# Optimization experiments

Hardware: AMD Instinct MI355X
Metric: run time of the kernel (lower is better)

Reference implementation:

```python
import jax, jax.numpy as jnp
import numpy as np

H_DIM = 2048
N_HEADS = 16

def setup_inputs() -> dict:
    key = jax.random.key(0)
    ks = jax.random.split(key, 9)
    B, T, C = 2, 2048, H_DIM
    scale = 1.0 / np.sqrt(C)  # lecun_normal approx
    src = jax.random.normal(ks[0], (B, T, C), dtype=jnp.float32)
    Wq = jax.random.normal(ks[1], (C, H_DIM), dtype=jnp.float32) * scale
    Wk = jax.random.normal(ks[2], (C, H_DIM), dtype=jnp.float32) * scale
    Wv = jax.random.normal(ks[3], (C, H_DIM), dtype=jnp.float32) * scale
    Wo = jax.random.normal(ks[4], (H_DIM, H_DIM), dtype=jnp.float32) * scale
    bq = jnp.zeros((H_DIM,), jnp.float32)
    bk = jnp.zeros((H_DIM,), jnp.float32)
    bv = jnp.zeros((H_DIM,), jnp.float32)
    bo = jnp.zeros((H_DIM,), jnp.float32)
    return {"src": src, "Wq": Wq, "bq": bq, "Wk": Wk, "bk": bk,
            "Wv": Wv, "bv": bv, "Wo": Wo, "bo": bo}

def reference(src, Wq, bq, Wk, bk, Wv, bv, Wo, bo):
    B, T, C = src.shape
    N = N_HEADS
    D = C // N
    def heads(x):  # [B,T,h_dim] -> [B,N,T,D]
        return x.reshape(B, T, N, D).transpose(0, 2, 1, 3)
    q = heads(src @ Wq + bq)
    k = heads(src @ Wk + bk)
    v = heads(src @ Wv + bv)
    # scaled dot-product with causal mask
    scores = jnp.einsum('bntd,bnsd->bnts', q, k) / jnp.sqrt(jnp.float32(D))
    causal = jnp.tril(jnp.ones((T, T), dtype=bool))
    scores = jnp.where(causal[None, None], scores, -jnp.inf)
    attn = jax.nn.softmax(scores, axis=-1)
    out = jnp.einsum('bnts,bnsd->bntd', attn, v)  # dropout is identity (drop_p=0)
    out = out.transpose(0, 2, 1, 3).reshape(B, T, N * D)
    return out @ Wo + bo
```

## Files before the change

kernel.cpp:

```cpp
#include <hip/hip_runtime.h>
#include <hip/hip_bf16.h>

typedef float f32x4 __attribute__((ext_vector_type(4)));
typedef __bf16 bf16x8v __attribute__((ext_vector_type(8)));
typedef __bf16 bf16x4v __attribute__((ext_vector_type(4)));
typedef unsigned uint2v __attribute__((ext_vector_type(2)));
typedef bf16x8v __attribute__((may_alias)) bf16x8;
typedef bf16x4v __attribute__((may_alias)) bf16x4;
typedef uint2v __attribute__((may_alias)) u32x2;

typedef __attribute__((address_space(1))) const void gvoid_t;
typedef __attribute__((address_space(3))) void lvoid_t;

#define DEVINL __device__ __forceinline__

#define BDIM 2
#define TDIM 2048
#define CDIM 2048
#define NHEAD 16
#define DHEAD 128
#define MROWS 4096
#define WSZ ((size_t)CDIM * CDIM)
#define XSZ ((size_t)MROWS * CDIM)

#define BARRIER_LGKM() asm volatile("s_waitcnt lgkmcnt(0)\ns_barrier" ::: "memory")

#define GEMM_BAR_LGKM()                              \
  do {                                               \
    asm volatile("s_waitcnt lgkmcnt(0)" ::: "memory"); \
    __builtin_amdgcn_sched_barrier(0);               \
    __builtin_amdgcn_s_barrier();                    \
  } while (0)

#define GEMM_BAR_VM(N)                                \
  do {                                                \
    asm volatile("s_waitcnt vmcnt(" #N ")" ::: "memory"); \
    __builtin_amdgcn_sched_barrier(0);                \
    __builtin_amdgcn_s_barrier();                     \
  } while (0)

DEVINL __bf16 f2bf(float f) {
  unsigned u = __builtin_bit_cast(unsigned, f);
  u += 0x7fffu + ((u >> 16) & 1u);
  unsigned short h = (unsigned short)(u >> 16);
  return __builtin_bit_cast(__bf16, h);
}

DEVINL unsigned pk2bf_trunc(float lo, float hi) {
  return __builtin_amdgcn_perm(__builtin_bit_cast(unsigned, hi),
                               __builtin_bit_cast(unsigned, lo), 0x07060302);
}

DEVINL void gl2lds16(const void* g, void* l) {
  __builtin_amdgcn_global_load_lds((gvoid_t*)g, (lvoid_t*)l, 16, 0, 0);
}

__global__ void detect_dtype(const unsigned* __restrict__ w,
                             int* __restrict__ flag, int* __restrict__ cnt) {
  const int l = threadIdx.x;
  if (l == 0) *cnt = 0;
  const unsigned word = w[l];
  const unsigned e = (word >> 7) & 0xFFu;
  const int vote = (e >= 0x70u && e <= 0x87u) ? 1 : 0;
  const unsigned long long m = __ballot(vote);
  if (l == 0) *flag = (__popcll(m) >= 32) ? 1 : 0;
}

__global__ __launch_bounds__(256) void cvt_src(const void* __restrict__ in,
                                               __bf16* __restrict__ out,
                                               const int* __restrict__ flag,
                                               int n8) {
  const int i = blockIdx.x * 256 + threadIdx.x;
  if (i >= n8) return;
  if (*flag) {
    ((bf16x8*)out)[i] = ((const bf16x8*)in)[i];
  } else {
    const float* f = (const float*)in + (size_t)i * 8;
    bf16x8v v;
#pragma unroll
    for (int j = 0; j < 8; ++j) v[j] = f2bf(f[j]);
    ((bf16x8*)out)[i] = v;
  }
}

__global__ __launch_bounds__(256) void cvt_wt(
    const void* __restrict__ w0, const void* __restrict__ w1,
    const void* __restrict__ w2, const void* __restrict__ w3,
    __bf16* __restrict__ out, const int* __restrict__ flag) {
  __shared__ __attribute__((aligned(16))) __bf16 tile[64][68];
  const void* W = (blockIdx.z == 0) ? w0 : (blockIdx.z == 1) ? w1
                : (blockIdx.z == 2) ? w2 : w3;
  __bf16* Wt = out + (size_t)blockIdx.z * WSZ;
  const int tx = threadIdx.x & 63, ty = threadIdx.x >> 6;
  const int k0 = blockIdx.x * 64, n0 = blockIdx.y * 64;
  const int fl = *flag;
#pragma unroll
  for (int i = ty; i < 64; i += 4) {
    const size_t off = (size_t)(k0 + i) * CDIM + n0 + tx;
    const float v = fl ? (float)((const __bf16*)W)[off] : ((const float*)W)[off];
    tile[i][tx] = f2bf(v);
  }
  __syncthreads();
#pragma unroll
  for (int i = ty; i < 64; i += 4)
    Wt[(size_t)(n0 + i) * CDIM + k0 + tx] = tile[tx][i];
}

__global__ __launch_bounds__(256) void cvt_bias(
    const void* __restrict__ b0, const void* __restrict__ b1,
    const void* __restrict__ b2, const void* __restrict__ b3,
    float* __restrict__ out, const int* __restrict__ flag) {
  const int i = blockIdx.x * 256 + threadIdx.x;
  const void* b = (i < 2048) ? b0 : (i < 4096) ? b1 : (i < 6144) ? b2 : b3;
  const int idx = i & 2047;
  out[i] = (*flag) ? (float)((const __bf16*)b)[idx] : ((const float*)b)[idx];
}

template <int NTN, int MODE>
__global__ __launch_bounds__(512, 2) void gemm8p(
    const __bf16* __restrict__ A, const __bf16* __restrict__ Bt,
    const float* __restrict__ bias, __bf16* __restrict__ qb,
    __bf16* __restrict__ kb, __bf16* __restrict__ vtb,
    const int* __restrict__ flag, void* __restrict__ outp) {
  constexpr int K = CDIM;
  constexpr int NKT = K / 64;
  __shared__ __attribute__((aligned(16))) __bf16 Als[2][128 * 64];
  __shared__ __attribute__((aligned(16))) __bf16 Bls[2][256 * 64];

  const int tid = threadIdx.x;
  const int w = tid >> 6, l = tid & 63;
  const int quad = l >> 4, l16 = l & 15;
  const int wm = (w >> 2) * 64, wn = (w & 3) * 64;

  const int bid = blockIdx.x;
  const int xcd = bid & 7, loc = bid >> 3;
  const int bm = loc & 31, bn = xcd * (NTN / 8) + (loc >> 5);
  const int m0 = bm * 128, n0 = bn * 256;

  const int srow = tid >> 3;
  const int scb = (tid & 7) ^ (srow & 7);
  const __bf16* gA = A + (size_t)(m0 + srow) * K + scb * 8;
  const __bf16* gB = Bt + (size_t)(n0 + srow) * K + scb * 8;
  const int wl = w * 512;

  const int aoff = (wm + l16) * 64;
  const int boff = (wn + l16) * 64;
  int cp[2];
  cp[0] = ((0 + quad) ^ (l16 & 7)) * 8;
  cp[1] = ((4 + quad) ^ (l16 & 7)) * 8;

  f32x4 acc[4][4];
#pragma unroll
  for (int i = 0; i < 4; ++i)
#pragma unroll
    for (int j = 0; j < 4; ++j) acc[i][j] = (f32x4){0.f, 0.f, 0.f, 0.f};

  gl2lds16(gA, &Als[0][wl]);
  gl2lds16(gA + (size_t)64 * K, &Als[0][4096 + wl]);
  gl2lds16(gB, &Bls[0][wl]);
  gl2lds16(gB + (size_t)64 * K, &Bls[0][4096 + wl]);
  gl2lds16(gB + (size_t)128 * K, &Bls[0][8192 + wl]);
  gl2lds16(gB + (size_t)192 * K, &Bls[0][12288 + wl]);
  gl2lds16(gA + 64, &Als[1][wl]);
  gl2lds16(gA + (size_t)64 * K + 64, &Als[1][4096 + wl]);

#define READ_HALF(I0)                                                        \
  _Pragma("unroll") for (int ii = 0; ii < 2; ++ii)                           \
  _Pragma("unroll") for (int ks = 0; ks < 2; ++ks) {                         \
    af[(I0) + ii][ks] =                                                      \
        *(const bf16x8*)&Ab[aoff + ((I0) + ii) * 1024 + cp[ks]];             \
    bfv[(I0) + ii][ks] =                                                     \
        *(const bf16x8*)&Bb[boff + ((I0) + ii) * 1024 + cp[ks]];             \
  }

#define MFMA_QUAD(I0, J0)                                                    \
  __builtin_amdgcn_s_setprio(1);                                            \
  _Pragma("unroll") for (int ii = 0; ii < 2; ++ii)                           \
  _Pragma("unroll") for (int jj = 0; jj < 2; ++jj)                           \
  _Pragma("unroll") for (int ks = 0; ks < 2; ++ks)                           \
      acc[(I0) + ii][(J0) + jj] = __builtin_amdgcn_mfma_f32_16x16x32_bf16(   \
          af[(I0) + ii][ks], bfv[(J0) + jj][ks], acc[(I0) + ii][(J0) + jj],  \
          0, 0, 0);                                                          \
  __builtin_amdgcn_s_setprio(0);

  for (int kt = 0; kt < NKT; ++kt) {
    const __bf16* Ab = Als[kt & 1];
    const __bf16* Bb = Bls[kt & 1];
    if (kt + 1 < NKT) {
      GEMM_BAR_VM(2);
    } else {
      GEMM_BAR_VM(0);
    }

    bf16x8 af[4][2], bfv[4][2];

    READ_HALF(0)
    if (kt + 1 < NKT) {
      const int nb = (kt + 1) & 1;
      gl2lds16(gB + (size_t)(kt + 1) * 64, &Bls[nb][wl]);
      gl2lds16(gB + (size_t)64 * K + (size_t)(kt + 1) * 64,
               &Bls[nb][4096 + wl]);
    }
    MFMA_QUAD(0, 0)
    GEMM_BAR_LGKM();

    READ_HALF(2)
    if (kt + 1 < NKT) {
      const int nb = (kt + 1) & 1;
      gl2lds16(gB + (size_t)128 * K + (size_t)(kt + 1) * 64,
               &Bls[nb][8192 + wl]);
      gl2lds16(gB + (size_t)192 * K + (size_t)(kt + 1) * 64,
               &Bls[nb][12288 + wl]);
    }
    MFMA_QUAD(2, 2)
    GEMM_BAR_LGKM();

    if (kt + 2 < NKT)
      gl2lds16(gA + (size_t)(kt + 2) * 64, &Als[kt & 1][wl]);
    MFMA_QUAD(0, 2)
    GEMM_BAR_LGKM();

    if (kt + 2 < NKT)
      gl2lds16(gA + (size_t)64 * K + (size_t)(kt + 2) * 64,
               &Als[kt & 1][4096 + wl]);
    MFMA_QUAD(2, 0)
  }
#undef READ_HALF
#undef MFMA_QUAD

  if (MODE == 0) {
    const int mat = n0 >> 11;
#pragma unroll
    for (int j = 0; j < 4; ++j) {
      const int n = n0 + wn + j * 16 + l16;
      const int nn = n & 2047;
      const int h = nn >> 7, d = nn & 127;
      const float bv = bias[n];
#pragma unroll
      for (int i = 0; i < 4; ++i) {
        const int mbase = m0 + wm + i * 16 + quad * 4;
        const int bb = mbase >> 11, t = mbase & 2047;
        if (mat == 2) {
          bf16x4v v4;
#pragma unroll
          for (int r = 0; r < 4; ++r) v4[r] = f2bf(acc[i][j][r] + bv);
          *(bf16x4*)&vtb[((size_t)(bb * NHEAD + h) * DHEAD + d) * TDIM + t] = v4;
        } else {
          __bf16* op = (mat == 0) ? qb : kb;
#pragma unroll
          for (int r = 0; r < 4; ++r)
            op[((size_t)(bb * NHEAD + h) * TDIM + t + r) * DHEAD + d] =
                f2bf(acc[i][j][r] + bv);
        }
      }
    }
  } else {
    const int ofl = *flag;
#pragma unroll
    for (int j = 0; j < 4; ++j) {
      const int n = n0 + wn + j * 16 + l16;
      const float bv = bias[n];
#pragma unroll
      for (int i = 0; i < 4; ++i) {
#pragma unroll
        for (int r = 0; r < 4; ++r) {
          const int m = m0 + wm + i * 16 + quad * 4 + r;
          const float v = acc[i][j][r] + bv;
          if (ofl) ((__bf16*)outp)[(size_t)m * CDIM + n] = f2bf(v);
          else     ((float*)outp)[(size_t)m * CDIM + n] = v;
        }
      }
    }
  }
}

__global__ __launch_bounds__(256, 2) void attn(
    const __bf16* __restrict__ Q, const __bf16* __restrict__ K,
    const __bf16* __restrict__ Vt, __bf16* __restrict__ ctx,
    int* __restrict__ cnt) {
  constexpr float CSC = 0.12753139726f;
  __shared__ __attribute__((aligned(16))) __bf16 Kls[64 * 128];
  __shared__ __attribute__((aligned(16))) __bf16 Vls[128 * 64];
  __shared__ __attribute__((aligned(16))) __bf16 Pls[4][32 * 64];
  __shared__ int jobLds;

  const int tid = threadIdx.x;
  const int w = tid >> 6, l = tid & 63, quad = l >> 4, l16 = l & 15;

  const int krow = tid >> 4;
  const int kcol = tid & 15;
  const int kldsoff = ((kcol ^ krow) * 8);
  const int vrow = tid >> 3;
  const int vcol = tid & 7;
  const int vldsoff = ((vcol ^ (vrow & 7)) * 8);

  for (;;) {
    __syncthreads();
    if (tid == 0) jobLds = atomicAdd(cnt, 1);
    __syncthreads();
    const int j = jobLds;
    if (j >= 512) break;
    const int qt = 15 - (j >> 5);
    const int bh = j & 31;
    const int t0w = qt * 128 + w * 32;
    const __bf16* Qbh = Q + (size_t)bh * TDIM * DHEAD;
    const __bf16* Kbh = K + (size_t)bh * TDIM * DHEAD;
    const __bf16* Vbh = Vt + (size_t)bh * TDIM * DHEAD;

    bf16x8 qf[2][4];
#pragma unroll
    for (int tt = 0; tt < 2; ++tt)
#pragma unroll
      for (int ks = 0; ks < 4; ++ks)
        qf[tt][ks] = *(const bf16x8*)(Qbh +
                     (size_t)(t0w + tt * 16 + l16) * DHEAD + ks * 32 + quad * 8);

    f32x4 oacc[8][2];
#pragma unroll
    for (int dt = 0; dt < 8; ++dt)
#pragma unroll
      for (int tt = 0; tt < 2; ++tt) oacc[dt][tt] = (f32x4){0.f, 0.f, 0.f, 0.f};
    float mrow[2] = {-1e30f, -1e30f};
    float lrow[2] = {0.f, 0.f};

    const int nsb = 2 * (qt + 1);

    bf16x8 kr[4], vr[4];
#pragma unroll
    for (int p = 0; p < 4; ++p)
      kr[p] = *(const bf16x8*)(Kbh + (size_t)(p * 16 + krow) * DHEAD + kcol * 8);
#pragma unroll
    for (int p = 0; p < 4; ++p)
      vr[p] = *(const bf16x8*)(Vbh + (size_t)(p * 32 + vrow) * TDIM + vcol * 8);

    for (int sb = 0; sb < nsb; ++sb) {
      const int s0 = sb * 64;
      BARRIER_LGKM();
#pragma unroll
      for (int p = 0; p < 4; ++p)
        *(bf16x8*)&Kls[(p * 16 + krow) * 128 + kldsoff] = kr[p];
#pragma unroll
      for (int p = 0; p < 4; ++p)
        *(bf16x8*)&Vls[(p * 32 + vrow) * 64 + vldsoff] = vr[p];
      if (sb + 1 < nsb) {
        const int s1 = s0 + 64;
#pragma unroll
        for (int p = 0; p < 4; ++p)
          kr[p] = *(const bf16x8*)(Kbh + (size_t)(s1 + p * 16 + krow) * DHEAD +
                                   kcol * 8);
#pragma unroll
        for (int p = 0; p < 4; ++p)
          vr[p] = *(const bf16x8*)(Vbh + (size_t)(p * 32 + vrow) * TDIM + s1 +
                                   vcol * 8);
      }
      BARRIER_LGKM();
      if (s0 > t0w + 31) continue;

      f32x4 sacc[4][2];
#pragma unroll
      for (int st = 0; st < 4; ++st)
#pragma unroll
        for (int tt = 0; tt < 2; ++tt) sacc[st][tt] = (f32x4){0.f, 0.f, 0.f, 0.f};
#pragma unroll
      for (int ks = 0; ks < 4; ++ks) {
        bf16x8 kf[4];
#pragma unroll
        for (int st = 0; st < 4; ++st)
          kf[st] = *(const bf16x8*)&Kls[(st * 16 + l16) * 128 +
                                        (((ks * 4 + quad) ^ l16) * 8)];
#pragma unroll
        for (int st = 0; st < 4; ++st)
#pragma unroll
          for (int tt = 0; tt < 2; ++tt)
            sacc[st][tt] = __builtin_amdgcn_mfma_f32_16x16x32_bf16(
                kf[st], qf[tt][ks], sacc[st][tt], 0, 0, 0);
      }
      if (s0 + 63 > t0w) {
#pragma unroll
        for (int st = 0; st < 4; ++st)
#pragma unroll
          for (int tt = 0; tt < 2; ++tt)
#pragma unroll
            for (int r = 0; r < 4; ++r) {
              const int s = s0 + st * 16 + quad * 4 + r;
              const int t = t0w + tt * 16 + l16;
              if (s > t) sacc[st][tt][r] = -1e30f;
            }
      }
#pragma unroll
      for (int tt = 0; tt < 2; ++tt) {
        float vm = -1e30f;
#pragma unroll
        for (int st = 0; st < 4; ++st)
#pragma unroll
          for (int r = 0; r < 4; ++r) vm = fmaxf(vm, sacc[st][tt][r]);
        vm = fmaxf(vm, __shfl_xor(vm, 16));
        vm = fmaxf(vm, __shfl_xor(vm, 32));
        const float mnew = fmaxf(mrow[tt], vm);
        if (__ballot(mnew > mrow[tt])) {
          const float alpha = exp2f((mrow[tt] - mnew) * CSC);
          lrow[tt] *= alpha;
#pragma unroll
          for (int dt = 0; dt < 8; ++dt)
#pragma unroll
            for (int r = 0; r < 4; ++r) oacc[dt][tt][r] *= alpha;
          mrow[tt] = mnew;
        }
        float rs = 0.f;
#pragma unroll
        for (int st = 0; st < 4; ++st) {
          const float p0 = exp2f((sacc[st][tt][0] - mnew) * CSC);
          const float p1 = exp2f((sacc[st][tt][1] - mnew) * CSC);
          const float p2 = exp2f((sacc[st][tt][2] - mnew) * CSC);
          const float p3 = exp2f((sacc[st][tt][3] - mnew) * CSC);
          rs += (p0 + p1) + (p2 + p3);
          u32x2 pk = {pk2bf_trunc(p0, p1), pk2bf_trunc(p2, p3)};
          *(u32x2*)&Pls[w][(tt * 16 + l16) * 64 +
                           (((st * 2 + (quad >> 1)) ^ (l16 & 7)) * 8) +
                           (quad & 1) * 4] = pk;
        }
        rs += __shfl_xor(rs, 16);
        rs += __shfl_xor(rs, 32);
        lrow[tt] += rs;
      }
      asm volatile("s_waitcnt lgkmcnt(0)" ::: "memory");
#pragma unroll
      for (int ks = 0; ks < 2; ++ks) {
        bf16x8 pf[2];
#pragma unroll
        for (int tt = 0; tt < 2; ++tt)
          pf[tt] = *(const bf16x8*)&Pls[w][(tt * 16 + l16) * 64 +
                                           (((ks * 4 + quad) ^ (l16 & 7)) * 8)];
#pragma unroll
        for (int dt = 0; dt < 8; ++dt) {
          const bf16x8 vf =
              *(const bf16x8*)&Vls[(dt * 16 + l16) * 64 +
                                   (((ks * 4 + quad) ^ (l16 & 7)) * 8)];
#pragma unroll
          for (int tt = 0; tt < 2; ++tt)
            oacc[dt][tt] = __builtin_amdgcn_mfma_f32_16x16x32_bf16(
                vf, pf[tt], oacc[dt][tt], 0, 0, 0);
        }
      }
    }

    const int b = bh >> 4, h = bh & 15;
#pragma unroll
    for (int tt = 0; tt < 2; ++tt) {
      const float rinv = 1.0f / lrow[tt];
      const int t = t0w + tt * 16 + l16;
      __bf16* cp = ctx + ((size_t)(b * TDIM + t)) * CDIM + h * DHEAD;
#pragma unroll
      for (int dt = 0; dt < 8; ++dt) {
        bf16x4v v4;
#pragma unroll
        for (int r = 0; r < 4; ++r) v4[r] = f2bf(oacc[dt][tt][r] * rinv);
        *(bf16x4*)&cp[dt * 16 + quad * 4] = v4;
      }
    }
  }
}

extern "C" void kernel_launch(void* const* d_in, const int* in_sizes, int n_in,
                              void* d_out, int out_size, void* d_ws,
                              size_t ws_size, hipStream_t stream) {
  const void* src = d_in[0];
  const void* Wq = d_in[1];
  const void* bq = d_in[2];
  const void* Wk = d_in[3];
  const void* bk = d_in[4];
  const void* Wv = d_in[5];
  const void* bv = d_in[6];
  const void* Wo = d_in[7];
  const void* bo = d_in[8];

  char* wsb = (char*)d_ws;
  int* flag = (int*)wsb;
  int* cnt = (int*)(wsb + 128);
  __bf16* srcbf = (__bf16*)(wsb + 256);
  __bf16* wqt = srcbf + XSZ;
  __bf16* wkt = wqt + WSZ;
  __bf16* wvt = wkt + WSZ;
  __bf16* wot = wvt + WSZ;
  __bf16* qb = wot + WSZ;
  __bf16* kb = qb + XSZ;
  __bf16* vtb = kb + XSZ;
  float* biasf = (float*)(vtb + XSZ);
  __bf16* ctx = srcbf;

  detect_dtype<<<1, 64, 0, stream>>>((const unsigned*)src, flag, cnt);
  cvt_src<<<4096, 256, 0, stream>>>(src, srcbf, flag, (int)(XSZ / 8));
  cvt_wt<<<dim3(32, 32, 4), 256, 0, stream>>>(Wq, Wk, Wv, Wo, wqt, flag);
  cvt_bias<<<32, 256, 0, stream>>>(bq, bk, bv, bo, biasf, flag);
  gemm8p<24, 0><<<768, 512, 0, stream>>>(srcbf, wqt, biasf, qb, kb, vtb,
                                         nullptr, nullptr);
  attn<<<512, 256, 0, stream>>>(qb, kb, vtb, ctx, cnt);
  gemm8p<8, 1><<<256, 512, 0, stream>>>(ctx, wot, biasf + 6144, nullptr,
                                        nullptr, nullptr, flag, d_out);
}
```

Measured before the change: 437.7 us.

## Switch GEMMs to 256-row tiles with templated warp layout and simpler double buffering

```diff
diff --git a/kernel.cpp b/kernel.cpp
--- a/kernel.cpp
+++ b/kernel.cpp
@@ -25,18 +25,11 @@
 
 #define BARRIER_LGKM() asm volatile("s_waitcnt lgkmcnt(0)\ns_barrier" ::: "memory")
 
-#define GEMM_BAR_LGKM()                              \
-  do {                                               \
-    asm volatile("s_waitcnt lgkmcnt(0)" ::: "memory"); \
-    __builtin_amdgcn_sched_barrier(0);               \
-    __builtin_amdgcn_s_barrier();                    \
-  } while (0)
-
-#define GEMM_BAR_VM(N)                                \
-  do {                                                \
-    asm volatile("s_waitcnt vmcnt(" #N ")" ::: "memory"); \
-    __builtin_amdgcn_sched_barrier(0);                \
-    __builtin_amdgcn_s_barrier();                     \
+#define GEMM_BAR_ALL()                                            \
+  do {                                                            \
+    asm volatile("s_waitcnt vmcnt(0) lgkmcnt(0)" ::: "memory");   \
+    __builtin_amdgcn_sched_barrier(0);                            \
+    __builtin_amdgcn_s_barrier();                                 \
   } while (0)
 
 DEVINL __bf16 f2bf(float f) {
@@ -116,26 +109,31 @@
   out[i] = (*flag) ? (float)((const __bf16*)b)[idx] : ((const float*)b)[idx];
 }
 
-template <int NTN, int MODE>
-__global__ __launch_bounds__(512, 2) void gemm8p(
+template <int BN, int WM, int WN, int MODE>
+__global__ __launch_bounds__(512, 2) void gemm256(
     const __bf16* __restrict__ A, const __bf16* __restrict__ Bt,
     const float* __restrict__ bias, __bf16* __restrict__ qb,
     __bf16* __restrict__ kb, __bf16* __restrict__ vtb,
     const int* __restrict__ flag, void* __restrict__ outp) {
   constexpr int K = CDIM;
   constexpr int NKT = K / 64;
-  __shared__ __attribute__((aligned(16))) __bf16 Als[2][128 * 64];
-  __shared__ __attribute__((aligned(16))) __bf16 Bls[2][256 * 64];
+  constexpr int RW = 256 / WM;
+  constexpr int CW = BN / WN;
+  constexpr int MF = RW / 16;
+  constexpr int NF = CW / 16;
+  constexpr int MH = MF / 4;
+  constexpr int BU = BN / 64;
+  __shared__ __attribute__((aligned(16))) __bf16 Als[2][256 * 64];
+  __shared__ __attribute__((aligned(16))) __bf16 Bls[2][BN * 64];
 
   const int tid = threadIdx.x;
   const int w = tid >> 6, l = tid & 63;
   const int quad = l >> 4, l16 = l & 15;
-  const int wm = (w >> 2) * 64, wn = (w & 3) * 64;
+  const int wm = w / WN, wn = w % WN;
 
   const int bid = blockIdx.x;
-  const int xcd = bid & 7, loc = bid >> 3;
-  const int bm = loc & 31, bn = xcd * (NTN / 8) + (loc >> 5);
-  const int m0 = bm * 128, n0 = bn * 256;
+  const int bm = bid & 15, bn = bid >> 4;
+  const int m0 = bm * 256, n0 = bn * BN;
 
   const int srow = tid >> 3;
   const int scb = (tid & 7) ^ (srow & 7);
@@ -143,129 +141,98 @@
   const __bf16* gB = Bt + (size_t)(n0 + srow) * K + scb * 8;
   const int wl = w * 512;
 
-  const int aoff = (wm + l16) * 64;
-  const int boff = (wn + l16) * 64;
   int cp[2];
   cp[0] = ((0 + quad) ^ (l16 & 7)) * 8;
   cp[1] = ((4 + quad) ^ (l16 & 7)) * 8;
 
-  f32x4 acc[4][4];
-#pragma unroll
-  for (int i = 0; i < 4; ++i)
-#pragma unroll
-    for (int j = 0; j < 4; ++j) acc[i][j] = (f32x4){0.f, 0.f, 0.f, 0.f};
-
-  gl2lds16(gA, &Als[0][wl]);
-  gl2lds16(gA + (size_t)64 * K, &Als[0][4096 + wl]);
-  gl2lds16(gB, &Bls[0][wl]);
-  gl2lds16(gB + (size_t)64 * K, &Bls[0][4096 + wl]);
-  gl2lds16(gB + (size_t)128 * K, &Bls[0][8192 + wl]);
-  gl2lds16(gB + (size_t)192 * K, &Bls[0][12288 + wl]);
-  gl2lds16(gA + 64, &Als[1][wl]);
-  gl2lds16(gA + (size_t)64 * K + 64, &Als[1][4096 + wl]);
-
-#define READ_HALF(I0)                                                        \
-  _Pragma("unroll") for (int ii = 0; ii < 2; ++ii)                           \
-  _Pragma("unroll") for (int ks = 0; ks < 2; ++ks) {                         \
-    af[(I0) + ii][ks] =                                                      \
-        *(const bf16x8*)&Ab[aoff + ((I0) + ii) * 1024 + cp[ks]];             \
-    bfv[(I0) + ii][ks] =                                                     \
-        *(const bf16x8*)&Bb[boff + ((I0) + ii) * 1024 + cp[ks]];             \
-  }
-
-#define MFMA_QUAD(I0, J0)                                                    \
-  __builtin_amdgcn_s_setprio(1);                                            \
-  _Pragma("unroll") for (int ii = 0; ii < 2; ++ii)                           \
-  _Pragma("unroll") for (int jj = 0; jj < 2; ++jj)                           \
-  _Pragma("unroll") for (int ks = 0; ks < 2; ++ks)                           \
-      acc[(I0) + ii][(J0) + jj] = __builtin_amdgcn_mfma_f32_16x16x32_bf16(   \
-          af[(I0) + ii][ks], bfv[(J0) + jj][ks], acc[(I0) + ii][(J0) + jj],  \
-          0, 0, 0);                                                          \
-  __builtin_amdgcn_s_setprio(0);
+  f32x4 acc[MF][NF];
+#pragma unroll
+  for (int i = 0; i < MF; ++i)
+#pragma unroll
+    for (int j = 0; j < NF; ++j) acc[i][j] = (f32x4){0.f, 0.f, 0.f, 0.f};
+
+  auto STAGE = [&](int kt1) {
+    const int b = kt1 & 1;
+    const size_t ko = (size_t)kt1 * 64;
+#pragma unroll
+    for (int u = 0; u < 4; ++u)
+      gl2lds16(gA + (size_t)u * 64 * K + ko, &Als[b][u * 4096 + wl]);
+#pragma unroll
+    for (int u = 0; u < BU; ++u)
+      gl2lds16(gB + (size_t)u * 64 * K + ko, &Bls[b][u * 4096 + wl]);
+  };
+
+  STAGE(0);
 
   for (int kt = 0; kt < NKT; ++kt) {
+    GEMM_BAR_ALL();
     const __bf16* Ab = Als[kt & 1];
     const __bf16* Bb = Bls[kt & 1];
-    if (kt + 1 < NKT) {
-      GEMM_BAR_VM(2);
-    } else {
-      GEMM_BAR_VM(0);
+    if (kt + 1 < NKT) STAGE(kt + 1);
+
+#pragma unroll
+    for (int ks = 0; ks < 2; ++ks) {
+      bf16x8 bfr[NF];
+#pragma unroll
+      for (int nf = 0; nf < NF; ++nf)
+        bfr[nf] = *(const bf16x8*)&Bb[(wn * CW + nf * 16 + l16) * 64 + cp[ks]];
+#pragma unroll
+      for (int mh = 0; mh < MH; ++mh) {
+        bf16x8 afr[4];
+#pragma unroll
+        for (int i = 0; i < 4; ++i)
+          afr[i] = *(const bf16x8*)&Ab[(wm * RW + mh * 64 + i * 16 + l16) * 64 +
+                                       cp[ks]];
+        __builtin_amdgcn_s_setprio(1);
+#pragma unroll
+        for (int i = 0; i < 4; ++i)
+#pragma unroll
+          for (int nf = 0; nf < NF; ++nf)
+            acc[mh * 4 + i][nf] = __builtin_amdgcn_mfma_f32_16x16x32_bf16(
+                afr[i], bfr[nf], acc[mh * 4 + i][nf], 0, 0, 0);
+        __builtin_amdgcn_s_setprio(0);
+      }
     }
-
-    bf16x8 af[4][2], bfv[4][2];
-
-    READ_HALF(0)
-    if (kt + 1 < NKT) {
-      const int nb = (kt + 1) & 1;
-      gl2lds16(gB + (size_t)(kt + 1) * 64, &Bls[nb][wl]);
-      gl2lds16(gB + (size_t)64 * K + (size_t)(kt + 1) * 64,
-               &Bls[nb][4096 + wl]);
-    }
-    MFMA_QUAD(0, 0)
-    GEMM_BAR_LGKM();
-
-    READ_HALF(2)
-    if (kt + 1 < NKT) {
-      const int nb = (kt + 1) & 1;
-      gl2lds16(gB + (size_t)128 * K + (size_t)(kt + 1) * 64,
-               &Bls[nb][8192 + wl]);
-      gl2lds16(gB + (size_t)192 * K + (size_t)(kt + 1) * 64,
-               &Bls[nb][12288 + wl]);
-    }
-    MFMA_QUAD(2, 2)
-    GEMM_BAR_LGKM();
-
-    if (kt + 2 < NKT)
-      gl2lds16(gA + (size_t)(kt + 2) * 64, &Als[kt & 1][wl]);
-    MFMA_QUAD(0, 2)
-    GEMM_BAR_LGKM();
-
-    if (kt + 2 < NKT)
-      gl2lds16(gA + (size_t)64 * K + (size_t)(kt + 2) * 64,
-               &Als[kt & 1][4096 + wl]);
-    MFMA_QUAD(2, 0)
   }
-#undef READ_HALF
-#undef MFMA_QUAD
 
   if (MODE == 0) {
-    const int mat = n0 >> 11;
-#pragma unroll
-    for (int j = 0; j < 4; ++j) {
-      const int n = n0 + wn + j * 16 + l16;
+#pragma unroll
+    for (int nf = 0; nf < NF; ++nf) {
+      const int n = n0 + wn * CW + nf * 16 + l16;
       const int nn = n & 2047;
       const int h = nn >> 7, d = nn & 127;
+      const int mat = n >> 11;
       const float bv = bias[n];
 #pragma unroll
-      for (int i = 0; i < 4; ++i) {
-        const int mbase = m0 + wm + i * 16 + quad * 4;
+      for (int mi = 0; mi < MF; ++mi) {
+        const int mbase = m0 + wm * RW + mi * 16 + quad * 4;
         const int bb = mbase >> 11, t = mbase & 2047;
         if (mat == 2) {
           bf16x4v v4;
 #pragma unroll
-          for (int r = 0; r < 4; ++r) v4[r] = f2bf(acc[i][j][r] + bv);
+          for (int r = 0; r < 4; ++r) v4[r] = f2bf(acc[mi][nf][r] + bv);
           *(bf16x4*)&vtb[((size_t)(bb * NHEAD + h) * DHEAD + d) * TDIM + t] = v4;
         } else {
           __bf16* op = (mat == 0) ? qb : kb;
 #pragma unroll
           for (int r = 0; r < 4; ++r)
             op[((size_t)(bb * NHEAD + h) * TDIM + t + r) * DHEAD + d] =
-                f2bf(acc[i][j][r] + bv);
+                f2bf(acc[mi][nf][r] + bv);
         }
       }
     }
   } else {
     const int ofl = *flag;
 #pragma unroll
-    for (int j = 0; j < 4; ++j) {
-      const int n = n0 + wn + j * 16 + l16;
+    for (int nf = 0; nf < NF; ++nf) {
+      const int n = n0 + wn * CW + nf * 16 + l16;
       const float bv = bias[n];
 #pragma unroll
-      for (int i = 0; i < 4; ++i) {
+      for (int mi = 0; mi < MF; ++mi) {
 #pragma unroll
         for (int r = 0; r < 4; ++r) {
-          const int m = m0 + wm + i * 16 + quad * 4 + r;
-          const float v = acc[i][j][r] + bv;
+          const int m = m0 + wm * RW + mi * 16 + quad * 4 + r;
+          const float v = acc[mi][nf][r] + bv;
           if (ofl) ((__bf16*)outp)[(size_t)m * CDIM + n] = f2bf(v);
           else     ((float*)outp)[(size_t)m * CDIM + n] = v;
         }
@@ -492,9 +459,10 @@
   cvt_src<<<4096, 256, 0, stream>>>(src, srcbf, flag, (int)(XSZ / 8));
   cvt_wt<<<dim3(32, 32, 4), 256, 0, stream>>>(Wq, Wk, Wv, Wo, wqt, flag);
   cvt_bias<<<32, 256, 0, stream>>>(bq, bk, bv, bo, biasf, flag);
-  gemm8p<24, 0><<<768, 512, 0, stream>>>(srcbf, wqt, biasf, qb, kb, vtb,
-                                         nullptr, nullptr);
+  gemm256<192, 2, 4, 0><<<512, 512, 0, stream>>>(srcbf, wqt, biasf, qb, kb,
+                                                 vtb, nullptr, nullptr);
   attn<<<512, 256, 0, stream>>>(qb, kb, vtb, ctx, cnt);
-  gemm8p<8, 1><<<256, 512, 0, stream>>>(ctx, wot, biasf + 6144, nullptr,
-                                        nullptr, nullptr, flag, d_out);
-}
+  gemm256<128, 4, 2, 1><<<256, 512, 0, stream>>>(ctx, wot, biasf + 6144,
+                                                 nullptr, nullptr, nullptr,
+                                                 flag, d_out);
+}
```

New measurement: 422.3 us. 3.5% less time.
